# Kernel tuning notes

Hardware: AMD Instinct MI355X
Metric: run time of the kernel (lower is better)

## Reference

```python
import jax, jax.numpy as jnp
import numpy as np

P, RES_H, RES_W = 32, 256, 256
H, W = 480, 640
FOCAL = 1.0


def setup_inputs() -> dict:
    key = jax.random.key(0)
    k1, k2, k3, k4 = jax.random.split(key, 4)
    # texture: alpha + rgb logits, uniform(-1,1) as in torch init
    plane_content = jax.random.uniform(k1, (P, 4, RES_H, RES_W), jnp.float32, -1.0, 1.0)
    # orthonormal plane basis (columns = plane x/y axes + normal)
    plane_basis, _ = jnp.linalg.qr(jax.random.normal(k2, (P, 3, 3), jnp.float32))
    xy = jax.random.normal(k3, (P, 2), jnp.float32)
    z = 2.0 + 4.0 * jax.random.uniform(k4, (P, 1), jnp.float32)  # planes in front of camera
    plane_position = jnp.concatenate([xy, z], axis=-1)
    plane_wh = jnp.full((P, 2), 2.0, jnp.float32)
    cam_R = jnp.eye(3, dtype=jnp.float32)   # world-to-cam rotation
    cam_T = jnp.zeros((3,), jnp.float32)    # world-to-cam translation
    return {"plane_content": plane_content, "plane_basis": plane_basis,
            "plane_position": plane_position, "plane_wh": plane_wh,
            "cam_R": cam_R, "cam_T": cam_T}


def _bilinear(img, uv):
    # img: (C, Hc, Wc); uv: (N, 2) in [-1, 1]. torch grid_sample bilinear,
    # align_corners=False, padding_mode='zeros'.
    C, Hc, Wc = img.shape
    x = (uv[:, 0] + 1.0) * Wc * 0.5 - 0.5
    y = (uv[:, 1] + 1.0) * Hc * 0.5 - 0.5
    x0 = jnp.floor(x)
    y0 = jnp.floor(y)
    wx = x - x0
    wy = y - y0

    def gather(xi, yi):
        inb = (xi >= 0) & (xi < Wc) & (yi >= 0) & (yi < Hc)
        xc = jnp.clip(xi, 0, Wc - 1).astype(jnp.int32)
        yc = jnp.clip(yi, 0, Hc - 1).astype(jnp.int32)
        return jnp.where(inb[None, :], img[:, yc, xc], 0.0)  # (C, N)

    v00 = gather(x0, y0)
    v01 = gather(x0 + 1.0, y0)
    v10 = gather(x0, y0 + 1.0)
    v11 = gather(x0 + 1.0, y0 + 1.0)
    top = v00 * (1.0 - wx) + v01 * wx
    bot = v10 * (1.0 - wx) + v11 * wx
    return (top * (1.0 - wy) + bot * wy).T  # (N, C)


def reference(plane_content, plane_basis, plane_position, plane_wh, cam_R, cam_T):
    N = H * W
    xs = ((jnp.arange(W, dtype=jnp.float32) + 0.5) / W) * 2.0 - 1.0
    ys = ((jnp.arange(H, dtype=jnp.float32) + 0.5) / H) * 2.0 - 1.0
    gy, gx = jnp.meshgrid(ys, xs, indexing='ij')
    # pinhole ray directions in camera frame (z-depth parameterization)
    dirs_cam = jnp.stack([gx.reshape(-1) / FOCAL, gy.reshape(-1) / FOCAL,
                          jnp.ones((N,), jnp.float32)], axis=-1)  # (N,3)
    cam_pos = -cam_R.T @ cam_T                 # camera center in world
    dirs_world = dirs_cam @ cam_R              # R^T d per ray, (N,3)

    normals = plane_basis[:, :, 2]             # (P,3)
    num = jnp.einsum('pc,pc->p', normals, plane_position - cam_pos[None])
    den = jnp.einsum('pc,nc->pn', normals, dirs_world)
    den = jnp.where(jnp.abs(den) < 1e-6, 1e-6, den)
    points_depth = num[:, None] / den          # (P,N) depth on each plane

    world_points = cam_pos[None, None] + points_depth[..., None] * dirs_world[None]  # (P,N,3)
    local = jnp.einsum('pnc,pcd->pnd', world_points - plane_position[:, None], plane_basis)
    uv = local[..., :2] / (plane_wh[:, None, :] * 0.5)        # normalize to [-1,1] inside plane
    in_planes = jnp.all(jnp.abs(uv) <= 1.0, axis=-1)          # (P,N)

    raw = jax.vmap(_bilinear)(plane_content, uv)              # (P,N,4)
    content = jnp.where(in_planes[..., None], jax.nn.sigmoid(raw), 0.0)

    sort_idx = jnp.argsort(points_depth, axis=0)              # front-to-back per pixel
    depth_sorted = jnp.take_along_axis(points_depth, sort_idx, axis=0)
    content_sorted = jnp.take_along_axis(content, sort_idx[..., None], axis=0)

    alpha = content_sorted[..., 0]                            # (P,N)
    color = content_sorted[..., 1:]                           # (P,N,3)
    trans = jnp.cumprod(1.0 - alpha, axis=0)
    trans = jnp.concatenate([jnp.ones((1, N), alpha.dtype), trans[:-1]], axis=0)
    weight = alpha * trans                                    # (P,N)

    depth_img = jnp.sum(depth_sorted * weight, axis=0).reshape(H, W)
    color_img = jnp.sum(color * weight[..., None], axis=0).reshape(H, W, 3)
    return jnp.concatenate([color_img, depth_img[..., None]], axis=-1)  # (H,W,4)
```

## Files before the change

kernel.cpp:

```cpp
#include <hip/hip_runtime.h>
#include <cstdint>

constexpr int P   = 32;
constexpr int RES = 256;
constexpr int H   = 480;
constexpr int W   = 640;
#define KMAX 0xFFFFFFFFu

__device__ __forceinline__ uint32_t mono_key(float f) {
    uint32_t b = __float_as_uint(f);
    return (b & 0x80000000u) ? ~b : (b | 0x80000000u);
}
__device__ __forceinline__ float unmono(uint32_t m) {
    uint32_t b = (m & 0x80000000u) ? (m ^ 0x80000000u) : ~m;
    return __uint_as_float(b);
}
__device__ __forceinline__ float h2f(unsigned short u) {
    return (float)__builtin_bit_cast(_Float16, u);
}
__device__ __forceinline__ unsigned short f2h(float f) {
    return __builtin_bit_cast(unsigned short, (_Float16)f);
}

__global__ __launch_bounds__(256) void prep_repack_kernel(
    const float* __restrict__ content,
    const float* __restrict__ basis, const float* __restrict__ ppos,
    const float* __restrict__ pwh,   const float* __restrict__ camR,
    const float* __restrict__ camT,
    float4* __restrict__ tab, ushort4* __restrict__ tex)
{
    const int tid = blockIdx.x * 256 + threadIdx.x;
    const float* src = content + (((size_t)(tid >> 16)) << 18) + (tid & 65535);
    ushort4 o;
    o.x = f2h(src[0]);
    o.y = f2h(src[65536]);
    o.z = f2h(src[131072]);
    o.w = f2h(src[196608]);
    tex[tid] = o;

    if (blockIdx.x == 0 && threadIdx.x < P) {
        const int p = threadIdx.x;
        const float T0=camT[0],T1=camT[1],T2=camT[2];
        const float cpx = -(camR[0]*T0 + camR[3]*T1 + camR[6]*T2);
        const float cpy = -(camR[1]*T0 + camR[4]*T1 + camR[7]*T2);
        const float cpz = -(camR[2]*T0 + camR[5]*T1 + camR[8]*T2);
        const float* b = basis + 9 * p;
        const float n0 = b[2], n1 = b[5], n2 = b[8];
        const float px = ppos[3*p], py = ppos[3*p+1], pz = ppos[3*p+2];
        const float num = n0*(px-cpx) + n1*(py-cpy) + n2*(pz-cpz);
        const float A0  = (cpx-px)*b[0] + (cpy-py)*b[3] + (cpz-pz)*b[6];
        const float A1  = (cpx-px)*b[1] + (cpy-py)*b[4] + (cpz-pz)*b[7];
        const float hw0 = pwh[2*p]   * 0.5f;
        const float hw1 = pwh[2*p+1] * 0.5f;
        tab[4*p+0] = make_float4(n0, n1, n2, num);
        tab[4*p+1] = make_float4(A0, A1, __int_as_float(p << 16), 0.f);
        tab[4*p+2] = make_float4(b[0], b[3], b[6], 1.0f/hw0);
        tab[4*p+3] = make_float4(b[1], b[4], b[7], 1.0f/hw1);
    }
}

__global__ __launch_bounds__(128, 2) void render_fast(
    const ushort4* __restrict__ tex, const float4* __restrict__ tab,
    const float* __restrict__ camR,  float* __restrict__ out)
{
    __shared__ float4 s_pl[P][3];

    const int t = threadIdx.x;
    if (t < P) {
        s_pl[t][0] = tab[4*t+1];
        s_pl[t][1] = tab[4*t+2];
        s_pl[t][2] = tab[4*t+3];
    }
    __syncthreads();

    const int x = blockIdx.x * 16 + (t & 15);
    const int y = blockIdx.y * 8 + (t >> 4);

    const float gx = ((float)x + 0.5f) / (float)W * 2.0f - 1.0f;
    const float gy = ((float)y + 0.5f) / (float)H * 2.0f - 1.0f;
    const float dwx = gx*camR[0] + gy*camR[3] + camR[6];
    const float dwy = gx*camR[1] + gy*camR[4] + camR[7];
    const float dwz = gx*camR[2] + gy*camR[5] + camR[8];

    uint32_t key[P];
    #pragma unroll
    for (int p = 0; p < P; ++p) {
        const float4 c0 = tab[4*p+0];
        const float4 c1 = tab[4*p+1];
        const float4 c2 = tab[4*p+2];
        const float4 c3 = tab[4*p+3];
        float den = c0.x*dwx + c0.y*dwy + c0.z*dwz;
        if (fabsf(den) < 1e-6f) den = 1e-6f;
        const float d  = c0.w / den;
        const float B0 = c2.x*dwx + c2.y*dwy + c2.z*dwz;
        const float B1 = c3.x*dwx + c3.y*dwy + c3.z*dwz;
        const float u  = (c1.x + d*B0) * c2.w;
        const float v  = (c1.y + d*B1) * c3.w;
        key[p] = (fabsf(u) <= 1.0f && fabsf(v) <= 1.0f) ? mono_key(d) : KMAX;
    }

    float aR = 0.f, aG = 0.f, aB = 0.f, aD = 0.f, tr = 1.f;

    auto argmin_pop = [&](int& obi) -> uint32_t {
        uint32_t bk = KMAX; int bi = 0;
        #pragma unroll
        for (int i = 0; i < P; ++i) {
            const bool c = key[i] < bk;
            bk = c ? key[i] : bk;
            bi = c ? i : bi;
        }
        #pragma unroll
        for (int i = 0; i < P; ++i)
            key[i] = (i == bi) ? KMAX : key[i];
        obi = bi;
        return bk;
    };

    struct St { ushort4 t00, t01, t10, t11; float d, wx, wy; int ix, iy; bool valid; };

    auto issue = [&](uint32_t k, int bi) -> St {
        St s;
        s.valid = (k != KMAX);
        const float d = s.valid ? unmono(k) : 0.0f;
        const float4 pA = s_pl[bi][0];
        const float4 pB = s_pl[bi][1];
        const float4 pC = s_pl[bi][2];
        const float B0 = pB.x*dwx + pB.y*dwy + pB.z*dwz;
        const float B1 = pC.x*dwx + pC.y*dwy + pC.z*dwz;
        const float u  = (pA.x + d*B0) * pB.w;
        const float v  = (pA.y + d*B1) * pC.w;
        const float fx = (u + 1.0f) * 128.0f - 0.5f;
        const float fy = (v + 1.0f) * 128.0f - 0.5f;
        const float x0f = floorf(fx), y0f = floorf(fy);
        s.wx = fx - x0f; s.wy = fy - y0f;
        s.ix = (int)x0f; s.iy = (int)y0f;
        s.d = d;
        const int x0c = min(max(s.ix,     0), RES-1);
        const int x1c = min(max(s.ix + 1, 0), RES-1);
        const int y0c = min(max(s.iy,     0), RES-1);
        const int y1c = min(max(s.iy + 1, 0), RES-1);
        const int base = __float_as_int(pA.z);
        const int r0 = base + (y0c << 8), r1 = base + (y1c << 8);
        s.t00 = tex[r0 + x0c]; s.t01 = tex[r0 + x1c];
        s.t10 = tex[r1 + x0c]; s.t11 = tex[r1 + x1c];
        return s;
    };

    auto consume = [&](const St& s) {
        ushort4 t00 = s.t00, t01 = s.t01, t10 = s.t10, t11 = s.t11;
        const bool mx0 = (uint32_t)s.ix       < (uint32_t)RES;
        const bool mx1 = (uint32_t)(s.ix + 1) < (uint32_t)RES;
        const bool my0 = (uint32_t)s.iy       < (uint32_t)RES;
        const bool my1 = (uint32_t)(s.iy + 1) < (uint32_t)RES;
        if (!(mx0 && my0)) { t00.x = t00.y = t00.z = t00.w = 0; }
        if (!(mx1 && my0)) { t01.x = t01.y = t01.z = t01.w = 0; }
        if (!(mx0 && my1)) { t10.x = t10.y = t10.z = t10.w = 0; }
        if (!(mx1 && my1)) { t11.x = t11.y = t11.z = t11.w = 0; }
        const float omwx = 1.0f - s.wx, omwy = 1.0f - s.wy;
        const unsigned short* q00 = (const unsigned short*)&t00;
        const unsigned short* q01 = (const unsigned short*)&t01;
        const unsigned short* q10 = (const unsigned short*)&t10;
        const unsigned short* q11 = (const unsigned short*)&t11;
        float c4[4];
        #pragma unroll
        for (int c = 0; c < 4; ++c) {
            const float top = h2f(q00[c]) * omwx + h2f(q01[c]) * s.wx;
            const float bot = h2f(q10[c]) * omwx + h2f(q11[c]) * s.wx;
            const float raw = top * omwy + bot * s.wy;
            c4[c] = __builtin_amdgcn_rcpf(1.0f + __expf(-raw));
        }
        const float a   = s.valid ? c4[0] : 0.0f;
        const float wgt = a * tr;
        aD += s.d * wgt;
        aR += c4[1] * wgt;
        aG += c4[2] * wgt;
        aB += c4[3] * wgt;
        tr *= (1.0f - a);
    };

    int cbi; uint32_t ck = argmin_pop(cbi);
    if (__ballot(ck != KMAX) != 0ull) {
        St cur = issue(ck, cbi);
        for (;;) {
            int nbi; const uint32_t nk = argmin_pop(nbi);
            const bool more = (__ballot(nk != KMAX) != 0ull);
            St nxt;
            if (more) nxt = issue(nk, nbi);
            consume(cur);
            if (!more) break;
            cur = nxt;
        }
    }

    const int o = (y * W + x) * 4;
    float4 res; res.x = aR; res.y = aG; res.z = aB; res.w = aD;
    *reinterpret_cast<float4*>(out + o) = res;
}

__global__ __launch_bounds__(256) void render_ref(
    const float* __restrict__ content, const float* __restrict__ basis,
    const float* __restrict__ ppos,    const float* __restrict__ pwh,
    const float* __restrict__ camR,    const float* __restrict__ camT,
    float* __restrict__ out)
{
    __shared__ float s_pl[P][20];
    const int t = threadIdx.x;
    const int x = blockIdx.x * 16 + (t & 15);
    const int y = blockIdx.y * 16 + (t >> 4);
    if (t < P) {
        const float* b = basis + t * 9;
        s_pl[t][0] = b[0]; s_pl[t][1] = b[3]; s_pl[t][2] = b[6];
        s_pl[t][3] = b[1]; s_pl[t][4] = b[4]; s_pl[t][5] = b[7];
        s_pl[t][6] = ppos[t*3+0]; s_pl[t][7] = ppos[t*3+1]; s_pl[t][8] = ppos[t*3+2];
        s_pl[t][9] = pwh[t*2+0] * 0.5f; s_pl[t][10] = pwh[t*2+1] * 0.5f;
    }
    __syncthreads();
    const float T0=camT[0],T1=camT[1],T2=camT[2];
    const float cpx = -(camR[0]*T0 + camR[3]*T1 + camR[6]*T2);
    const float cpy = -(camR[1]*T0 + camR[4]*T1 + camR[7]*T2);
    const float cpz = -(camR[2]*T0 + camR[5]*T1 + camR[8]*T2);
    const float gx = ((float)x + 0.5f) / (float)W * 2.0f - 1.0f;
    const float gy = ((float)y + 0.5f) / (float)H * 2.0f - 1.0f;
    const float dwx = gx*camR[0] + gy*camR[3] + camR[6];
    const float dwy = gx*camR[1] + gy*camR[4] + camR[7];
    const float dwz = gx*camR[2] + gy*camR[5] + camR[8];
    uint32_t key[P];
    #pragma unroll
    for (int p = 0; p < P; ++p) {
        const float b00=basis[p*9+0], b01=basis[p*9+1], n0=basis[p*9+2];
        const float b10=basis[p*9+3], b11=basis[p*9+4], n1=basis[p*9+5];
        const float b20=basis[p*9+6], b21=basis[p*9+7], n2=basis[p*9+8];
        const float px=ppos[p*3+0], py=ppos[p*3+1], pz=ppos[p*3+2];
        const float hw0=pwh[p*2+0]*0.5f, hw1=pwh[p*2+1]*0.5f;
        const float num = n0*(px-cpx) + n1*(py-cpy) + n2*(pz-cpz);
        float den = n0*dwx + n1*dwy + n2*dwz;
        if (fabsf(den) < 1e-6f) den = 1e-6f;
        const float depth = num / den;
        const float ox = cpx + depth*dwx - px;
        const float oy = cpy + depth*dwy - py;
        const float oz = cpz + depth*dwz - pz;
        const float u = (ox*b00 + oy*b10 + oz*b20) / hw0;
        const float v = (ox*b01 + oy*b11 + oz*b21) / hw1;
        key[p] = (fabsf(u) <= 1.0f && fabsf(v) <= 1.0f) ? mono_key(depth) : KMAX;
    }
    float aR=0.f,aG=0.f,aB=0.f,aD=0.f,tr=1.f;
    #pragma unroll 1
    for (int it = 0; it < P; ++it) {
        uint32_t bk = KMAX; int bi = 0;
        #pragma unroll
        for (int i = 0; i < P; ++i) {
            const bool c = key[i] < bk;
            bk = c ? key[i] : bk; bi = c ? i : bi;
        }
        if (bk == KMAX) break;
        #pragma unroll
        for (int i = 0; i < P; ++i) key[i] = (i == bi) ? KMAX : key[i];
        const float depth = unmono(bk);
        const float* pl = s_pl[bi];
        const float ox = cpx + depth*dwx - pl[6];
        const float oy = cpy + depth*dwy - pl[7];
        const float oz = cpz + depth*dwz - pl[8];
        const float u = (ox*pl[0] + oy*pl[1] + oz*pl[2]) / pl[9];
        const float v = (ox*pl[3] + oy*pl[4] + oz*pl[5]) / pl[10];
        const float fx = (u + 1.0f) * 128.0f - 0.5f;
        const float fy = (v + 1.0f) * 128.0f - 0.5f;
        const float x0f = floorf(fx), y0f = floorf(fy);
        const float wx = fx - x0f, wy = fy - y0f;
        const int ix = (int)x0f, iy = (int)y0f;
        const int x0c = min(max(ix,0),RES-1), x1c = min(max(ix+1,0),RES-1);
        const int y0c = min(max(iy,0),RES-1), y1c = min(max(iy+1,0),RES-1);
        const float m00 = ((uint32_t)ix<(uint32_t)RES && (uint32_t)iy<(uint32_t)RES) ? 1.f:0.f;
        const float m01 = ((uint32_t)(ix+1)<(uint32_t)RES && (uint32_t)iy<(uint32_t)RES) ? 1.f:0.f;
        const float m10 = ((uint32_t)ix<(uint32_t)RES && (uint32_t)(iy+1)<(uint32_t)RES) ? 1.f:0.f;
        const float m11 = ((uint32_t)(ix+1)<(uint32_t)RES && (uint32_t)(iy+1)<(uint32_t)RES) ? 1.f:0.f;
        const int o00=y0c*RES+x0c, o01=y0c*RES+x1c, o10=y1c*RES+x0c, o11=y1c*RES+x1c;
        const float* pc = content + ((size_t)bi << 18);
        float c4[4];
        #pragma unroll
        for (int c = 0; c < 4; ++c) {
            const float* ic = pc + (c << 16);
            const float v00 = ic[o00]*m00, v01 = ic[o01]*m01;
            const float v10 = ic[o10]*m10, v11 = ic[o11]*m11;
            const float top = v00*(1.f-wx) + v01*wx;
            const float bot = v10*(1.f-wx) + v11*wx;
            const float raw = top*(1.f-wy) + bot*wy;
            c4[c] = 1.0f / (1.0f + __expf(-raw));
        }
        const float wgt = c4[0]*tr;
        aD += depth*wgt; aR += c4[1]*wgt; aG += c4[2]*wgt; aB += c4[3]*wgt;
        tr *= (1.0f - c4[0]);
    }
    const int o = (y * W + x) * 4;
    float4 res; res.x=aR; res.y=aG; res.z=aB; res.w=aD;
    *reinterpret_cast<float4*>(out + o) = res;
}

extern "C" void kernel_launch(void* const* d_in, const int* in_sizes, int n_in,
                              void* d_out, int out_size, void* d_ws, size_t ws_size,
                              hipStream_t stream) {
    const float* content = (const float*)d_in[0];
    const float* basis   = (const float*)d_in[1];
    const float* ppos    = (const float*)d_in[2];
    const float* pwh     = (const float*)d_in[3];
    const float* camR    = (const float*)d_in[4];
    const float* camT    = (const float*)d_in[5];

    const size_t TAB_BYTES = 2048;
    const size_t need = TAB_BYTES + (size_t)P * 65536 * sizeof(ushort4);

    if (ws_size >= need) {
        float4*  tab = (float4*)d_ws;
        ushort4* tex = (ushort4*)((char*)d_ws + TAB_BYTES);
        prep_repack_kernel<<<P * 65536 / 256, 256, 0, stream>>>(
            content, basis, ppos, pwh, camR, camT, tab, tex);
        render_fast<<<dim3(W / 16, H / 8), dim3(128), 0, stream>>>(
            tex, tab, camR, (float*)d_out);
    } else {
        dim3 grid(W / 16, H / 16);
        render_ref<<<grid, dim3(256), 0, stream>>>(
            content, basis, ppos, pwh, camR, camT, (float*)d_out);
    }
}
```

Baseline: 36.86 us.

## Batch four sorted planes per iteration to overlap texture gathers

Replaces the one-ahead software pipeline with a loop that pops four nearest planes, issues all sixteen texture loads, then composites them in order. Out-of-bounds masks are precomputed into a flag word at issue time, and invalid slots load from a safe address. The launch-bounds occupancy hint is dropped to give the compiler more registers. This aims to hide gather latency with more loads in flight, at the cost of higher register pressure and extra wasted work when a pixel's plane count is not a multiple of four.

```diff
diff --git a/kernel.cpp b/kernel.cpp
--- a/kernel.cpp
+++ b/kernel.cpp
@@ -59,7 +59,7 @@
     }
 }
 
-__global__ __launch_bounds__(128, 2) void render_fast(
+__global__ __launch_bounds__(128) void render_fast(
     const ushort4* __restrict__ tex, const float4* __restrict__ tab,
     const float* __restrict__ camR,  float* __restrict__ out)
 {
@@ -101,7 +101,7 @@
 
     float aR = 0.f, aG = 0.f, aB = 0.f, aD = 0.f, tr = 1.f;
 
-    auto argmin_pop = [&](int& obi) -> uint32_t {
+    auto pop1 = [&](uint32_t& ok, int& obi) {
         uint32_t bk = KMAX; int bi = 0;
         #pragma unroll
         for (int i = 0; i < P; ++i) {
@@ -112,16 +112,15 @@
         #pragma unroll
         for (int i = 0; i < P; ++i)
             key[i] = (i == bi) ? KMAX : key[i];
-        obi = bi;
-        return bk;
+        ok = bk; obi = bi;
     };
 
-    struct St { ushort4 t00, t01, t10, t11; float d, wx, wy; int ix, iy; bool valid; };
-
-    auto issue = [&](uint32_t k, int bi) -> St {
-        St s;
-        s.valid = (k != KMAX);
-        const float d = s.valid ? unmono(k) : 0.0f;
+    struct Slot { float d, wx, wy; int fl; ushort4 t00, t01, t10, t11; };
+
+    auto issue = [&](uint32_t k, int bi) -> Slot {
+        Slot s;
+        const bool valid = (k != KMAX);
+        const float d = valid ? unmono(k) : 0.0f;
         const float4 pA = s_pl[bi][0];
         const float4 pB = s_pl[bi][1];
         const float4 pC = s_pl[bi][2];
@@ -132,30 +131,33 @@
         const float fx = (u + 1.0f) * 128.0f - 0.5f;
         const float fy = (v + 1.0f) * 128.0f - 0.5f;
         const float x0f = floorf(fx), y0f = floorf(fy);
-        s.wx = fx - x0f; s.wy = fy - y0f;
-        s.ix = (int)x0f; s.iy = (int)y0f;
-        s.d = d;
-        const int x0c = min(max(s.ix,     0), RES-1);
-        const int x1c = min(max(s.ix + 1, 0), RES-1);
-        const int y0c = min(max(s.iy,     0), RES-1);
-        const int y1c = min(max(s.iy + 1, 0), RES-1);
-        const int base = __float_as_int(pA.z);
+        s.wx = fx - x0f; s.wy = fy - y0f; s.d = d;
+        const int ix = (int)x0f, iy = (int)y0f;
+        const bool mx0 = (uint32_t)ix       < (uint32_t)RES;
+        const bool mx1 = (uint32_t)(ix + 1) < (uint32_t)RES;
+        const bool my0 = (uint32_t)iy       < (uint32_t)RES;
+        const bool my1 = (uint32_t)(iy + 1) < (uint32_t)RES;
+        s.fl = (mx0 && my0 ? 1 : 0) | (mx1 && my0 ? 2 : 0)
+             | (mx0 && my1 ? 4 : 0) | (mx1 && my1 ? 8 : 0)
+             | (valid ? 16 : 0);
+        int x0c = min(max(ix,     0), RES-1);
+        int x1c = min(max(ix + 1, 0), RES-1);
+        int y0c = min(max(iy,     0), RES-1);
+        int y1c = min(max(iy + 1, 0), RES-1);
+        int base = __float_as_int(pA.z);
+        if (!valid) { base = 0; x0c = x1c = y0c = y1c = 0; }
         const int r0 = base + (y0c << 8), r1 = base + (y1c << 8);
         s.t00 = tex[r0 + x0c]; s.t01 = tex[r0 + x1c];
         s.t10 = tex[r1 + x0c]; s.t11 = tex[r1 + x1c];
         return s;
     };
 
-    auto consume = [&](const St& s) {
+    auto consume = [&](const Slot& s) {
         ushort4 t00 = s.t00, t01 = s.t01, t10 = s.t10, t11 = s.t11;
-        const bool mx0 = (uint32_t)s.ix       < (uint32_t)RES;
-        const bool mx1 = (uint32_t)(s.ix + 1) < (uint32_t)RES;
-        const bool my0 = (uint32_t)s.iy       < (uint32_t)RES;
-        const bool my1 = (uint32_t)(s.iy + 1) < (uint32_t)RES;
-        if (!(mx0 && my0)) { t00.x = t00.y = t00.z = t00.w = 0; }
-        if (!(mx1 && my0)) { t01.x = t01.y = t01.z = t01.w = 0; }
-        if (!(mx0 && my1)) { t10.x = t10.y = t10.z = t10.w = 0; }
-        if (!(mx1 && my1)) { t11.x = t11.y = t11.z = t11.w = 0; }
+        if (!(s.fl & 1)) { t00.x = t00.y = t00.z = t00.w = 0; }
+        if (!(s.fl & 2)) { t01.x = t01.y = t01.z = t01.w = 0; }
+        if (!(s.fl & 4)) { t10.x = t10.y = t10.z = t10.w = 0; }
+        if (!(s.fl & 8)) { t11.x = t11.y = t11.z = t11.w = 0; }
         const float omwx = 1.0f - s.wx, omwy = 1.0f - s.wy;
         const unsigned short* q00 = (const unsigned short*)&t00;
         const unsigned short* q01 = (const unsigned short*)&t01;
@@ -169,7 +171,7 @@
             const float raw = top * omwy + bot * s.wy;
             c4[c] = __builtin_amdgcn_rcpf(1.0f + __expf(-raw));
         }
-        const float a   = s.valid ? c4[0] : 0.0f;
+        const float a   = (s.fl & 16) ? c4[0] : 0.0f;
         const float wgt = a * tr;
         aD += s.d * wgt;
         aR += c4[1] * wgt;
@@ -178,18 +180,19 @@
         tr *= (1.0f - a);
     };
 
-    int cbi; uint32_t ck = argmin_pop(cbi);
-    if (__ballot(ck != KMAX) != 0ull) {
-        St cur = issue(ck, cbi);
-        for (;;) {
-            int nbi; const uint32_t nk = argmin_pop(nbi);
-            const bool more = (__ballot(nk != KMAX) != 0ull);
-            St nxt;
-            if (more) nxt = issue(nk, nbi);
-            consume(cur);
-            if (!more) break;
-            cur = nxt;
-        }
+    for (;;) {
+        uint32_t k0, k1, k2, k3; int b0, b1, b2, b3;
+        pop1(k0, b0); pop1(k1, b1); pop1(k2, b2); pop1(k3, b3);
+        if (__ballot(k0 != KMAX) == 0ull) break;
+        Slot s0 = issue(k0, b0);
+        Slot s1 = issue(k1, b1);
+        Slot s2 = issue(k2, b2);
+        Slot s3 = issue(k3, b3);
+        consume(s0);
+        consume(s1);
+        consume(s2);
+        consume(s3);
+        if (__ballot(k3 != KMAX) == 0ull) break;
     }
 
     const int o = (y * W + x) * 4;
```

New measurement: 40.07 us. 8.7% more time.

## Split planes across two waves per pixel tile and merge sorted samples via LDS

Applied to the files above, without the earlier changes.

Each 128-thread block now covers a 16x4 pixel tile, with each of its two waves handling 16 of the 32 planes for the same 64 pixels. Each wave sorts and samples only its half of the planes and writes depth keys and fp16-packed sigmoid colours into shared memory. After a barrier, a two-way merge composites the samples front to back for each pixel. This halves the per-thread key array and shortens the argmin sort loops, doubles the block count, and drops the occupancy hint. The cost is extra LDS traffic, a merge phase where half of each wave's lanes sit idle, and rounding sigmoid outputs to fp16.

```diff
diff --git a/kernel.cpp b/kernel.cpp
--- a/kernel.cpp
+++ b/kernel.cpp
@@ -59,36 +59,44 @@
     }
 }
 
-__global__ __launch_bounds__(128, 2) void render_fast(
+__global__ __launch_bounds__(128) void render_fast(
     const ushort4* __restrict__ tex, const float4* __restrict__ tab,
     const float* __restrict__ camR,  float* __restrict__ out)
 {
-    __shared__ float4 s_pl[P][3];
-
-    const int t = threadIdx.x;
+    __shared__ float4   s_pl[P][3];
+    __shared__ uint32_t s_key[2][16][64];
+    __shared__ uint2    s_c4 [2][16][64];
+
+    const int t    = threadIdx.x;
+    const int lane = t & 63;
+    const int w    = t >> 6;
+
     if (t < P) {
         s_pl[t][0] = tab[4*t+1];
         s_pl[t][1] = tab[4*t+2];
         s_pl[t][2] = tab[4*t+3];
     }
+    #pragma unroll
+    for (int e = 0; e < 16; ++e) s_key[w][e][lane] = KMAX;
     __syncthreads();
 
-    const int x = blockIdx.x * 16 + (t & 15);
-    const int y = blockIdx.y * 8 + (t >> 4);
-
+    const int x = blockIdx.x * 16 + (lane & 15);
+    const int y = blockIdx.y * 4  + (lane >> 4);
     const float gx = ((float)x + 0.5f) / (float)W * 2.0f - 1.0f;
     const float gy = ((float)y + 0.5f) / (float)H * 2.0f - 1.0f;
     const float dwx = gx*camR[0] + gy*camR[3] + camR[6];
     const float dwy = gx*camR[1] + gy*camR[4] + camR[7];
     const float dwz = gx*camR[2] + gy*camR[5] + camR[8];
 
-    uint32_t key[P];
+    const int pb = __builtin_amdgcn_readfirstlane(w) * 16;
+
+    uint32_t key[16];
     #pragma unroll
-    for (int p = 0; p < P; ++p) {
-        const float4 c0 = tab[4*p+0];
-        const float4 c1 = tab[4*p+1];
-        const float4 c2 = tab[4*p+2];
-        const float4 c3 = tab[4*p+3];
+    for (int p = 0; p < 16; ++p) {
+        const float4 c0 = tab[4*(pb+p)+0];
+        const float4 c1 = tab[4*(pb+p)+1];
+        const float4 c2 = tab[4*(pb+p)+2];
+        const float4 c3 = tab[4*(pb+p)+3];
         float den = c0.x*dwx + c0.y*dwy + c0.z*dwz;
         if (fabsf(den) < 1e-6f) den = 1e-6f;
         const float d  = c0.w / den;
@@ -99,32 +107,32 @@
         key[p] = (fabsf(u) <= 1.0f && fabsf(v) <= 1.0f) ? mono_key(d) : KMAX;
     }
 
-    float aR = 0.f, aG = 0.f, aB = 0.f, aD = 0.f, tr = 1.f;
-
     auto argmin_pop = [&](int& obi) -> uint32_t {
         uint32_t bk = KMAX; int bi = 0;
         #pragma unroll
-        for (int i = 0; i < P; ++i) {
+        for (int i = 0; i < 16; ++i) {
             const bool c = key[i] < bk;
             bk = c ? key[i] : bk;
             bi = c ? i : bi;
         }
         #pragma unroll
-        for (int i = 0; i < P; ++i)
+        for (int i = 0; i < 16; ++i)
             key[i] = (i == bi) ? KMAX : key[i];
         obi = bi;
         return bk;
     };
 
-    struct St { ushort4 t00, t01, t10, t11; float d, wx, wy; int ix, iy; bool valid; };
+    struct St { ushort4 t00, t01, t10, t11; float wx, wy; int ix, iy; uint32_t key; };
 
     auto issue = [&](uint32_t k, int bi) -> St {
         St s;
-        s.valid = (k != KMAX);
-        const float d = s.valid ? unmono(k) : 0.0f;
-        const float4 pA = s_pl[bi][0];
-        const float4 pB = s_pl[bi][1];
-        const float4 pC = s_pl[bi][2];
+        s.key = k;
+        const bool valid = (k != KMAX);
+        const float d = valid ? unmono(k) : 0.0f;
+        const int g = pb + bi;
+        const float4 pA = s_pl[g][0];
+        const float4 pB = s_pl[g][1];
+        const float4 pC = s_pl[g][2];
         const float B0 = pB.x*dwx + pB.y*dwy + pB.z*dwz;
         const float B1 = pC.x*dwx + pC.y*dwy + pC.z*dwz;
         const float u  = (pA.x + d*B0) * pB.w;
@@ -134,7 +142,6 @@
         const float x0f = floorf(fx), y0f = floorf(fy);
         s.wx = fx - x0f; s.wy = fy - y0f;
         s.ix = (int)x0f; s.iy = (int)y0f;
-        s.d = d;
         const int x0c = min(max(s.ix,     0), RES-1);
         const int x1c = min(max(s.ix + 1, 0), RES-1);
         const int y0c = min(max(s.iy,     0), RES-1);
@@ -146,7 +153,8 @@
         return s;
     };
 
-    auto consume = [&](const St& s) {
+    auto store = [&](const St& s, int e) {
+        if (s.key == KMAX) return;
         ushort4 t00 = s.t00, t01 = s.t01, t10 = s.t10, t11 = s.t11;
         const bool mx0 = (uint32_t)s.ix       < (uint32_t)RES;
         const bool mx1 = (uint32_t)(s.ix + 1) < (uint32_t)RES;
@@ -169,15 +177,13 @@
             const float raw = top * omwy + bot * s.wy;
             c4[c] = __builtin_amdgcn_rcpf(1.0f + __expf(-raw));
         }
-        const float a   = s.valid ? c4[0] : 0.0f;
-        const float wgt = a * tr;
-        aD += s.d * wgt;
-        aR += c4[1] * wgt;
-        aG += c4[2] * wgt;
-        aB += c4[3] * wgt;
-        tr *= (1.0f - a);
+        s_key[w][e][lane] = s.key;
+        s_c4[w][e][lane]  = make_uint2(
+            (uint32_t)f2h(c4[0]) | ((uint32_t)f2h(c4[1]) << 16),
+            (uint32_t)f2h(c4[2]) | ((uint32_t)f2h(c4[3]) << 16));
     };
 
+    int e = 0;
     int cbi; uint32_t ck = argmin_pop(cbi);
     if (__ballot(ck != KMAX) != 0ull) {
         St cur = issue(ck, cbi);
@@ -186,15 +192,47 @@
             const bool more = (__ballot(nk != KMAX) != 0ull);
             St nxt;
             if (more) nxt = issue(nk, nbi);
-            consume(cur);
+            store(cur, e); ++e;
             if (!more) break;
             cur = nxt;
         }
     }
-
-    const int o = (y * W + x) * 4;
-    float4 res; res.x = aR; res.y = aG; res.z = aB; res.w = aD;
-    *reinterpret_cast<float4*>(out + o) = res;
+    __syncthreads();
+
+    const int q  = w * 32 + (t & 31);
+    const bool act = (t & 63) < 32;
+    int i0 = 0, i1 = 0;
+    uint32_t k0 = act ? s_key[0][0][q] : KMAX;
+    uint32_t k1 = act ? s_key[1][0][q] : KMAX;
+    float aR = 0.f, aG = 0.f, aB = 0.f, aD = 0.f, tr = 1.f;
+
+    while (__ballot(k0 != KMAX || k1 != KMAX) != 0ull) {
+        const bool take0 = (k0 <= k1);
+        const uint32_t k = take0 ? k0 : k1;
+        const bool valid = (k != KMAX);
+        const int  li = (take0 ? i0 : i1) & 15;
+        const uint2 cp = s_c4[take0 ? 0 : 1][li][q];
+        if (take0) { ++i0; k0 = (i0 < 16) ? s_key[0][i0][q] : KMAX; }
+        else       { ++i1; k1 = (i1 < 16) ? s_key[1][i1][q] : KMAX; }
+        const float a  = valid ? h2f((unsigned short)(cp.x & 0xFFFFu)) : 0.0f;
+        const float cR = valid ? h2f((unsigned short)(cp.x >> 16))     : 0.0f;
+        const float cG = valid ? h2f((unsigned short)(cp.y & 0xFFFFu)) : 0.0f;
+        const float cB = valid ? h2f((unsigned short)(cp.y >> 16))     : 0.0f;
+        const float d  = valid ? unmono(k) : 0.0f;
+        const float wgt = a * tr;
+        aD += d  * wgt;
+        aR += cR * wgt;
+        aG += cG * wgt;
+        aB += cB * wgt;
+        tr *= (1.0f - a);
+    }
+
+    if (act) {
+        const int px = blockIdx.x * 16 + (q & 15);
+        const int py = blockIdx.y * 4  + (q >> 4);
+        float4 res; res.x = aR; res.y = aG; res.z = aB; res.w = aD;
+        *reinterpret_cast<float4*>(out + (py * W + px) * 4) = res;
+    }
 }
 
 __global__ __launch_bounds__(256) void render_ref(
@@ -313,7 +351,7 @@
         ushort4* tex = (ushort4*)((char*)d_ws + TAB_BYTES);
         prep_repack_kernel<<<P * 65536 / 256, 256, 0, stream>>>(
             content, basis, ppos, pwh, camR, camT, tab, tex);
-        render_fast<<<dim3(W / 16, H / 8), dim3(128), 0, stream>>>(
+        render_fast<<<dim3(W / 16, H / 4), dim3(128), 0, stream>>>(
             tex, tab, camR, (float*)d_out);
     } else {
         dim3 grid(W / 16, H / 16);
```

After: 35.65 us, median of 2. -3.3%, faster.
